# Kernel tuning notes

Measured on AMD Instinct MI355X. Metric: run time of the kernel, lower is better.

## Reference

```python
import jax, jax.numpy as jnp
import numpy as np

DIM = 256
HEADS = 8
HEAD_DIM = 32
INNER = HEADS * HEAD_DIM  # 256
B, L_AG, H, W = 2, 5, 32, 32
SEQ = H * W
POS_HID = 32


def _lin(k, fan_in, fan_out):
    kw, kb = jax.random.split(k)
    Wt = jax.random.normal(kw, (fan_in, fan_out), jnp.float32) * (fan_in ** -0.5)
    b = jax.random.normal(kb, (fan_out,), jnp.float32) * 0.01
    return Wt, b


def setup_inputs() -> dict:
    key = jax.random.key(0)
    ks = jax.random.split(key, 10)
    x = jax.random.normal(ks[0], (B, L_AG, H, W, DIM), jnp.float32)
    Wq, bq = _lin(ks[1], DIM, INNER)
    Wk, bk = _lin(ks[2], DIM, INNER)
    Wv, bv = _lin(ks[3], DIM, INNER)
    Wp1, bp1 = _lin(ks[4], 3, POS_HID)
    Wp2, bp2 = _lin(ks[5], POS_HID, HEADS)
    Ws1, bs1 = _lin(ks[6], DIM, POS_HID)
    Ws2, bs2 = _lin(ks[7], POS_HID, HEADS)
    Wo, bo = _lin(ks[8], INNER, DIM)
    Wg, bg = _lin(ks[9], 2 * DIM, DIM)
    return dict(x=x, Wq=Wq, bq=bq, Wk=Wk, bk=bk, Wv=Wv, bv=bv,
                Wp1=Wp1, bp1=bp1, Wp2=Wp2, bp2=bp2,
                Ws1=Ws1, bs1=bs1, Ws2=Ws2, bs2=bs2,
                Wo=Wo, bo=bo, Wg=Wg, bg=bg)


def _relative_positions(h, w):
    # coords: (h*w, 2), row-major (i//w, i%w) like torch meshgrid 'ij'
    yy, xx = jnp.meshgrid(jnp.arange(h), jnp.arange(w), indexing='ij')
    coords = jnp.stack([yy.reshape(-1), xx.reshape(-1)], axis=-1)  # (L,2)
    rel = (coords[:, None, :] - coords[None, :, :]).astype(jnp.float32)  # (L,L,2)
    dist = jnp.linalg.norm(rel, axis=-1, keepdims=True)  # (L,L,1)
    return jnp.concatenate([rel, dist], axis=-1)  # (L,L,3)


def reference(x, Wq, bq, Wk, bk, Wv, bv, Wp1, bp1, Wp2, bp2,
              Ws1, bs1, Ws2, bs2, Wo, bo, Wg, bg):
    b, l, h, w, c = x.shape
    bl, L = b * l, h * w
    scale = HEAD_DIM ** -0.5
    x2 = x.reshape(bl, L, c)

    q = (x2 @ Wq + bq).reshape(bl, L, HEADS, HEAD_DIM)
    k = (x2 @ Wk + bk).reshape(bl, L, HEADS, HEAD_DIM)
    v = (x2 @ Wv + bv).reshape(bl, L, HEADS, HEAD_DIM)

    scores = jnp.einsum('bihd,bjhd->bhij', q, k) * scale  # (bl,H,L,L)

    rel_pos = _relative_positions(h, w)  # (L,L,3)
    pos_w = jax.nn.relu(rel_pos @ Wp1 + bp1) @ Wp2 + bp2  # (L,L,heads)
    pos_w = jnp.transpose(pos_w, (2, 0, 1))[None]  # (1,heads,L,L)

    s = jax.nn.relu(x2 @ Ws1 + bs1) @ Ws2 + bs2  # (bl,L,heads)
    fsim = jnp.einsum('bih,bjh->bij', s, s)[:, None]  # (bl,1,L,L)

    probs = jax.nn.softmax(scores + pos_w + fsim, axis=-1)
    out = jnp.einsum('bhij,bjhd->bihd', probs, v).reshape(bl, L, INNER)
    out = out @ Wo + bo  # (bl,L,dim); dropout is identity in eval

    gate = jax.nn.sigmoid(jnp.concatenate([x2, out], axis=-1) @ Wg + bg)
    out = gate * out + (1.0 - gate) * x2
    return out.reshape(b, l, h, w, c)
```

## Files before the change

### kernel.cpp

```cpp
#include <hip/hip_runtime.h>

typedef __bf16 bf16_t;
typedef __bf16 bf16x4 __attribute__((ext_vector_type(4)));
typedef __bf16 bf16x8 __attribute__((ext_vector_type(8)));
typedef float  f32x4  __attribute__((ext_vector_type(4)));

#define HEADS 8
#define HEAD_DIM 32
#define DIM 256
#define BL 10
#define SEQ 1024
#define M_TOTAL (BL*SEQ)
#define QK_SCALE 0.17677669529663687f
#define LOG2E 1.4426950408889634f
#define SQRT_LOG2E 1.2011224087864498f
#define NPOS (63*63)

#define NCAST 2596
#define NTRANS 96
#define NPREP (NCAST + NTRANS + 16)

__device__ __forceinline__ int swz_idx(int row, int col) {
  return row*64 + (col ^ ((row & 7) << 3));
}
// ... 20 lines not shown
  if (bid < NCAST) {
    const int NX4 = M_TOTAL*DIM/4;
    const int i = bid*256 + tid;
    if (i < NX4) {
      const float4 v = ((const float4*)x)[i];
      bf16x4 o; o[0]=(bf16_t)v.x; o[1]=(bf16_t)v.y; o[2]=(bf16_t)v.z; o[3]=(bf16_t)v.w;
      *(bf16x4*)(xb + (size_t)i*4) = o;
      return;
    }
    int idx = i - NX4;
    if (idx < 8192) {
      const int m = idx >> 8, k = idx & 255;
      btall[(768 + m)*256 + k] = (bf16_t)Ws1[k*32 + m];
      return;
    }
    idx -= 8192;
    if (idx < 832) {
      bias_all[idx] = (idx < 256) ? bq[idx] : (idx < 512) ? bk[idx-256] :
                      (idx < 768) ? bv[idx-512] : (idx < 800) ? bs1[idx-768] : 0.f;
    }
    return;
  }

  if (bid < NCAST + NTRANS) {
    const int t0 = bid - NCAST;
    const int z = t0 >> 4, bi = (t0 & 15) >> 2, bj = t0 & 3;
    const float* src; bf16_t* dst;
    switch (z) {
      case 0: src = Wq;          dst = btall;          break;
      case 1: src = Wk;          dst = btall + 65536;  break;
      case 2: src = Wv;          dst = btall + 131072; break;
      case 3: src = Wo;          dst = wot;            break;
      case 4: src = Wg;          dst = wg1t;           break;
      default: src = Wg + 65536; dst = wg2t;           break;
    }
    const int tr = tid >> 4, tc = tid & 15;
    #pragma unroll
    for (int i = 0; i < 4; ++i) {
      const float4 v = *(const float4*)(src + (size_t)(bi*64 + tr + 16*i)*256 + bj*64 + tc*4);
      float* tp = &tile[tr + 16*i][tc*4];
      tp[0]=v.x; tp[1]=v.y; tp[2]=v.z; tp[3]=v.w;
    }
    __syncthreads();
    #pragma unroll
    for (int i = 0; i < 4; ++i) {
      bf16x4 o;
      #pragma unroll
      for (int e = 0; e < 4; ++e) o[e] = (bf16_t)tile[tc*4 + e][tr + 16*i];
      *(bf16x4*)(dst + (size_t)(bj*64 + tr + 16*i)*256 + bi*64 + tc*4) = o;
    }
    return;
  }

  {
    float* sm = &tile[0][0];
    float* w1 = sm; float* b1 = sm + 96; float* w2 = sm + 128; float* b2 = sm + 384;
    if (tid < 96) w1[tid] = Wp1[tid];
    if (tid < 32) b1[tid] = bp1[tid];
    w2[tid] = Wp2[tid];
    if (tid < 8)  b2[tid] = bp2[tid];
    __syncthreads();
    const int p = (bid - NCAST - NTRANS)*256 + tid;
    if (p >= NPOS) return;
    const float dy = (float)(p / 63 - 31);
    const float dx = (float)(p % 63 - 31);
    const float dist = sqrtf(dy*dy + dx*dx);
    float o[8];
    #pragma unroll
    for (int t = 0; t < 8; ++t) o[t] = b2[t];
    #pragma unroll
    for (int m = 0; m < 32; ++m) {
      float hv = fmaf(dy, w1[m], fmaf(dx, w1[32+m], fmaf(dist, w1[64+m], b1[m])));
      hv = fmaxf(hv, 0.f);
      #pragma unroll
      for (int t = 0; t < 8; ++t) o[t] = fmaf(hv, w2[m*8+t], o[t]);
    }
    #pragma unroll
    for (int t = 0; t < 8; ++t) posT[t*NPOS + p] = o[t]*LOG2E;
  }
}

__global__ __launch_bounds__(256) void qkv_kernel(
    const bf16_t* __restrict__ xb, const bf16_t* __restrict__ btall,
    const float* __restrict__ bias_all,
    bf16_t* __restrict__ qbuf, bf16_t* __restrict__ kbuf, bf16_t* __restrict__ vbuf,
    float* __restrict__ hidf)
{
  const int mt = blockIdx.x, ngb = blockIdx.y;
  const int tid = threadIdx.x;
  const int w = tid >> 6, lane = tid & 63, g = lane >> 4, l15 = lane & 15;
  const int arow = mt*64 + w*16 + l15;
  const bf16x8* Arow = (const bf16x8*)(xb + (size_t)arow*DIM);
  bf16x8 af[8];
  #pragma unroll
  for (int kc = 0; kc < 8; ++kc) af[kc] = Arow[kc*4 + g];
  const bool ishid = (ngb == 12);
  const int cmax = ishid ? 2 : 4;
  bf16_t* dst = (ngb < 4) ? qbuf : (ngb < 8) ? kbuf : vbuf;
  const int coloff = (ngb & 3) * 64;
  const float scale = (ngb < 4) ? QK_SCALE*LOG2E : 1.f;
  for (int c = 0; c < cmax; ++c) {
    const int n = ngb*64 + c*16 + l15;
    const bf16x8* Brow = (const bf16x8*)(btall + (size_t)n*DIM);
    f32x4 acc = {0.f,0.f,0.f,0.f};
    #pragma unroll
    for (int kc = 0; kc < 8; ++kc)
      acc = __builtin_amdgcn_mfma_f32_16x16x32_bf16(af[kc], Brow[kc*4+g], acc, 0, 0, 0);
    const float bvv = bias_all[n];
    #pragma unroll
    for (int r = 0; r < 4; ++r) {
      const int row = mt*64 + w*16 + g*4 + r;
      const float val = acc[r] + bvv;
      if (ishid) hidf[(size_t)row*32 + c*16 + l15] = fmaxf(val, 0.f);
      else dst[(size_t)row*DIM + coloff + c*16 + l15] = (bf16_t)(val*scale);
    }
  }
}

__global__ __launch_bounds__(256) void s2_kernel(
    const float* __restrict__ hidf, const float* __restrict__ Ws2,
    const float* __restrict__ bs2, float* __restrict__ sf)
{
  const int row = blockIdx.x*blockDim.x + threadIdx.x;
  if (row >= M_TOTAL) return;
  const float4* h4 = (const float4*)(hidf + (size_t)row*32);
  float sv[8];
  #pragma unroll
  for (int t = 0; t < 8; ++t) sv[t] = bs2[t];
  #pragma unroll
  for (int mq = 0; mq < 8; ++mq) {
    const float4 h = h4[mq];
    const float hv[4] = {h.x, h.y, h.z, h.w};
    #pragma unroll
    for (int e = 0; e < 4; ++e) {
      #pragma unroll
      for (int t = 0; t < 8; ++t) sv[t] = fmaf(hv[e], Ws2[(mq*4+e)*8+t], sv[t]);
    }
  }
  #pragma unroll
  for (int t = 0; t < 8; ++t) sf[(size_t)row*8+t] = sv[t]*SQRT_LOG2E;
}

__global__ __launch_bounds__(256) void attn_kernel(
    const bf16_t* __restrict__ qb, const bf16_t* __restrict__ kb,
    const bf16_t* __restrict__ vb, const float* __restrict__ sf,
    const float* __restrict__ posT, bf16_t* __restrict__ att)
{
  __shared__ __align__(16) bf16_t lqp[64*64];
  __shared__ __align__(16) bf16_t lk[64*64];
  __shared__ __align__(16) bf16_t lv[48*64];

  const int wg = blockIdx.x;
  const int xcd = wg & 7, within = wg >> 3;
  const int pair = xcd*10 + (within >> 4);
  const int it = within & 15;
  const int h = pair & 7, b = pair >> 3;
  const int i0 = it*64;
  const int tid = threadIdx.x;
  const int w = tid >> 6, lane = tid & 63, g = lane >> 4, l15 = lane & 15;
  const int r4 = tid >> 2, q4 = tid & 3;

  const float* posTh = posT + h*NPOS;
  int Cr[4];
  #pragma unroll
  for (int r = 0; r < 4; ++r) {
    const int irow = i0 + w*16 + g*4 + r;
    Cr[r] = ((irow >> 5) + 31)*63 + (irow & 31) + 31;
  }

  bf16x8 kreg = *(const bf16x8*)(kb + (size_t)(b*SEQ + r4)*DIM + h*HEAD_DIM + q4*8);
  bf16x8 vreg = *(const bf16x8*)(vb + (size_t)(b*SEQ + r4)*DIM + h*HEAD_DIM + q4*8);
  float4 sA, sB;
  if (tid < 64) {
    const float* sp = sf + (size_t)(b*SEQ + tid)*8;
    sA = *(const float4*)sp; sB = *(const float4*)(sp + 4);
  }
  float pf[4][4];
  #pragma unroll
  for (int c = 0; c < 4; ++c) {
    const int j = c*16 + l15;
    const int gj = (j >> 5)*63 + (j & 31);
    #pragma unroll
    for (int r = 0; r < 4; ++r) pf[c][r] = posTh[Cr[r] - gj];
  }

  for (int p = tid; p < 16*64; p += 256) {
    const int d = 32 + (p >> 6), j = p & 63;
    lv[d*64 + (j ^ ((d & 7) << 3))] = (bf16_t)((d == 32) ? 1.f : 0.f);
  }
  for (int p = tid; p < 192; p += 256) {
    const int rr = p / 3, ch = 5 + (p % 3);
    bf16x8 z;
    #pragma unroll
    for (int e = 0; e < 8; ++e) z[e] = (bf16_t)0.f;
    *(bf16x8*)&lk[swz_idx(rr, ch*8)] = z;
  }
  {
    const int grow = b*SEQ + i0 + r4;
    #pragma unroll
    for (int cc = 0; cc < 2; ++cc) {
      const int ch = q4*2 + cc;
      bf16x8 v;
      if (ch < 4) {
        v = *(const bf16x8*)(qb + (size_t)grow*DIM + h*HEAD_DIM + ch*8);
      } else if (ch == 4) {
        const float* sp = sf + (size_t)grow*8;
        #pragma unroll
        for (int e = 0; e < 8; ++e) v[e] = (bf16_t)sp[e];
      } else {
        #pragma unroll
        for (int e = 0; e < 8; ++e) v[e] = (bf16_t)0.f;
      }
      *(bf16x8*)&lqp[swz_idx(r4, ch*8)] = v;
    }
  }
  __syncthreads();

  const int qrow = w*16 + l15;
  const bf16x8 aq0 = *(const bf16x8*)&lqp[swz_idx(qrow, g*8)];
  const bf16x8 aq1 = *(const bf16x8*)&lqp[swz_idx(qrow, 32 + g*8)];

  f32x4 accO0 = {0.f,0.f,0.f,0.f}, accO1 = {0.f,0.f,0.f,0.f}, accO2 = {0.f,0.f,0.f,0.f};
  float mrow[4];
  #pragma unroll
  for (int r = 0; r < 4; ++r) mrow[r] = -1e30f;

  for (int jt = 0; jt < 16; ++jt) {
    const int j0 = jt*64;
    __syncthreads();
    *(bf16x8*)&lk[swz_idx(r4, q4*8)] = kreg;
    #pragma unroll
    for (int e = 0; e < 8; ++e) {
      const int d = q4*8 + e;
      lv[d*64 + (r4 ^ ((d & 7) << 3))] = vreg[e];
    }
    if (tid < 64) {
      bf16x8 sv;
      sv[0]=(bf16_t)sA.x; sv[1]=(bf16_t)sA.y; sv[2]=(bf16_t)sA.z; sv[3]=(bf16_t)sA.w;
      sv[4]=(bf16_t)sB.x; sv[5]=(bf16_t)sB.y; sv[6]=(bf16_t)sB.z; sv[7]=(bf16_t)sB.w;
      *(bf16x8*)&lk[swz_idx(tid, 32)] = sv;
    }
    __syncthreads();

    if (jt < 15) {
      const int grow = b*SEQ + j0 + 64 + r4;
      kreg = *(const bf16x8*)(kb + (size_t)grow*DIM + h*HEAD_DIM + q4*8);
      vreg = *(const bf16x8*)(vb + (size_t)grow*DIM + h*HEAD_DIM + q4*8);
      if (tid < 64) {
        const float* sp = sf + (size_t)(b*SEQ + j0 + 64 + tid)*8;
        sA = *(const float4*)sp; sB = *(const float4*)(sp + 4);
      }
    }

    f32x4 s4[4];
    #pragma unroll
    for (int c = 0; c < 4; ++c) {
      const int krow = c*16 + l15;
      const bf16x8 bk0 = *(const bf16x8*)&lk[swz_idx(krow, g*8)];
      const bf16x8 bk1 = *(const bf16x8*)&lk[swz_idx(krow, 32 + g*8)];
      f32x4 acc = {0.f,0.f,0.f,0.f};
      acc = __builtin_amdgcn_mfma_f32_16x16x32_bf16(aq0, bk0, acc, 0, 0, 0);
      acc = __builtin_amdgcn_mfma_f32_16x16x32_bf16(aq1, bk1, acc, 0, 0, 0);
      s4[c] = acc;
    }

    #pragma unroll
    for (int c = 0; c < 4; ++c) {
      #pragma unroll
      for (int r = 0; r < 4; ++r) s4[c][r] += pf[c][r];
    }
    if (jt < 15) {
      #pragma unroll
      for (int c = 0; c < 4; ++c) {
        const int j = j0 + 64 + c*16 + l15;
        const int gj = (j >> 5)*63 + (j & 31);
        #pragma unroll
        for (int r = 0; r < 4; ++r) pf[c][r] = posTh[Cr[r] - gj];
      }
    }

    float pmax[4];
    #pragma unroll
    for (int r = 0; r < 4; ++r)
      pmax[r] = fmaxf(fmaxf(s4[0][r], s4[1][r]), fmaxf(s4[2][r], s4[3][r]));
    #pragma unroll
    for (int mk = 1; mk <= 8; mk <<= 1) {
      #pragma unroll
      for (int r = 0; r < 4; ++r)
        pmax[r] = fmaxf(pmax[r], __shfl_xor(pmax[r], mk));
    }
    bool need = false;
    #pragma unroll
    for (int r = 0; r < 4; ++r) need = need || (pmax[r] > mrow[r] + 8.f);
    if (__any(need)) {
      #pragma unroll
      for (int r = 0; r < 4; ++r) {
        const float mn = fmaxf(mrow[r], pmax[r]);
        const float alpha = exp2f(mrow[r] - mn);
        mrow[r] = mn;
        accO0[r] *= alpha; accO1[r] *= alpha; accO2[r] *= alpha;
      }
    }
    #pragma unroll
    for (int r = 0; r < 4; ++r) {
      #pragma unroll
      for (int c = 0; c < 4; ++c) s4[c][r] = exp2f(s4[c][r] - mrow[r]);
    }

    #pragma unroll
    for (int c = 0; c < 4; ++c) {
      #pragma unroll
      for (int r = 0; r < 4; ++r)
        lqp[swz_idx(w*16 + g*4 + r, c*16 + l15)] = (bf16_t)s4[c][r];
    }

    const int prow = w*16 + l15;
    #pragma unroll
    for (int kc = 0; kc < 2; ++kc) {
      const bf16x8 ap  = *(const bf16x8*)&lqp[swz_idx(prow, kc*32 + g*8)];
      const bf16x8 bv0 = *(const bf16x8*)&lv[swz_idx(l15,      kc*32 + g*8)];
      const bf16x8 bv1 = *(const bf16x8*)&lv[swz_idx(16 + l15, kc*32 + g*8)];
      const bf16x8 bv2 = *(const bf16x8*)&lv[swz_idx(32 + l15, kc*32 + g*8)];
      accO0 = __builtin_amdgcn_mfma_f32_16x16x32_bf16(ap, bv0, accO0, 0, 0, 0);
      accO1 = __builtin_amdgcn_mfma_f32_16x16x32_bf16(ap, bv1, accO1, 0, 0, 0);
      accO2 = __builtin_amdgcn_mfma_f32_16x16x32_bf16(ap, bv2, accO2, 0, 0, 0);
    }
  }

  #pragma unroll
  for (int r = 0; r < 4; ++r) {
    const int row = b*SEQ + i0 + w*16 + g*4 + r;
    const float lsum = __shfl(accO2[r], lane & 48);
    const float inv = 1.f / lsum;
    att[(size_t)row*DIM + h*HEAD_DIM + l15]      = (bf16_t)(accO0[r]*inv);
    att[(size_t)row*DIM + h*HEAD_DIM + 16 + l15] = (bf16_t)(accO1[r]*inv);
  }
}

__global__ __launch_bounds__(256) void prjgate_kernel(
    const bf16_t* __restrict__ att, const bf16_t* __restrict__ wot,
    const float* __restrict__ bo, const bf16_t* __restrict__ xb,
    const float* __restrict__ x, const bf16_t* __restrict__ wg1t,
    const bf16_t* __restrict__ wg2t, const float* __restrict__ bg,
    float* __restrict__ outp)
{
  __shared__ __align__(16) bf16_t prjT[16*256];
  const int row0 = blockIdx.x * 16;
  const int tid = threadIdx.x;
  const int w = tid >> 6, lane = tid & 63, g = lane >> 4, l15 = lane & 15;
  const int arow = row0 + l15;

  {
    const bf16x8* Arow = (const bf16x8*)(att + (size_t)arow*DIM);
    bf16x8 afA[8];
    #pragma unroll
    for (int kc = 0; kc < 8; ++kc) afA[kc] = Arow[kc*4 + g];
    #pragma unroll
    for (int ct = 0; ct < 4; ++ct) {
      const int n = w*64 + ct*16 + l15;
      const bf16x8* Brow = (const bf16x8*)(wot + (size_t)n*DIM);
      f32x4 acc = {0.f,0.f,0.f,0.f};
      #pragma unroll
      for (int kc = 0; kc < 8; ++kc)
        acc = __builtin_amdgcn_mfma_f32_16x16x32_bf16(afA[kc], Brow[kc*4+g], acc, 0, 0, 0);
      const float bvo = bo[n];
      #pragma unroll
      for (int r = 0; r < 4; ++r)
        prjT[swz256(g*4 + r, n)] = (bf16_t)(acc[r] + bvo);
    }
  }
  __syncthreads();

  const bf16x8* A1r = (const bf16x8*)(xb + (size_t)arow*DIM);
  bf16x8 a1[8], a2[8];
  #pragma unroll
  for (int kc = 0; kc < 8; ++kc) {
    a1[kc] = A1r[kc*4 + g];
    a2[kc] = *(const bf16x8*)&prjT[swz256(l15, kc*32 + g*8)];
  }
  #pragma unroll
  for (int ct = 0; ct < 4; ++ct) {
    const int n = w*64 + ct*16 + l15;
    const bf16x8* b1 = (const bf16x8*)(wg1t + (size_t)n*DIM);
    const bf16x8* b2 = (const bf16x8*)(wg2t + (size_t)n*DIM);
    f32x4 acc = {0.f,0.f,0.f,0.f};
    #pragma unroll
    for (int kc = 0; kc < 8; ++kc)
      acc = __builtin_amdgcn_mfma_f32_16x16x32_bf16(a1[kc], b1[kc*4+g], acc, 0, 0, 0);
    #pragma unroll
    for (int kc = 0; kc < 8; ++kc)
      acc = __builtin_amdgcn_mfma_f32_16x16x32_bf16(a2[kc], b2[kc*4+g], acc, 0, 0, 0);
    const float bgv = bg[n];
    #pragma unroll
    for (int r = 0; r < 4; ++r) {
      const int grow = row0 + g*4 + r;
      const float gate = 1.f / (1.f + __expf(-(acc[r] + bgv)));
      const float pv = (float)prjT[swz256(g*4 + r, n)];
      const float xv = x[(size_t)grow*DIM + n];
      outp[(size_t)grow*DIM + n] = gate*pv + (1.f - gate)*xv;
    }
  }
}

extern "C" void kernel_launch(void* const* d_in, const int* in_sizes, int n_in,
                              void* d_out, int out_size, void* d_ws, size_t ws_size,
                              hipStream_t stream)
{
  const float* x   = (const float*)d_in[0];
  const float* Wq  = (const float*)d_in[1];
  const float* bq  = (const float*)d_in[2];
  const float* Wk  = (const float*)d_in[3];
  const float* bk  = (const float*)d_in[4];
  const float* Wv  = (const float*)d_in[5];
  const float* bv  = (const float*)d_in[6];
  const float* Wp1 = (const float*)d_in[7];
  const float* bp1 = (const float*)d_in[8];
  const float* Wp2 = (const float*)d_in[9];
  const float* bp2 = (const float*)d_in[10];
  const float* Ws1 = (const float*)d_in[11];
  const float* bs1 = (const float*)d_in[12];
  const float* Ws2 = (const float*)d_in[13];
  const float* bs2 = (const float*)d_in[14];
  const float* Wo  = (const float*)d_in[15];
  const float* bo  = (const float*)d_in[16];
  const float* Wg  = (const float*)d_in[17];
  const float* bg  = (const float*)d_in[18];

  char* ws = (char*)d_ws;
  size_t off = 0;
  auto alloc = [&](size_t bytes) {
    char* p = ws + off;
    off += (bytes + 255) & ~(size_t)255;
    return p;
  };
  bf16_t* xb    = (bf16_t*)alloc((size_t)M_TOTAL*DIM*2);
  bf16_t* qbuf  = (bf16_t*)alloc((size_t)M_TOTAL*DIM*2);
  bf16_t* kbuf  = (bf16_t*)alloc((size_t)M_TOTAL*DIM*2);
  bf16_t* vbuf  = (bf16_t*)alloc((size_t)M_TOTAL*DIM*2);
  bf16_t* att   = (bf16_t*)alloc((size_t)M_TOTAL*DIM*2);
  bf16_t* btall = (bf16_t*)alloc((size_t)800*256*2);
  bf16_t* wot   = (bf16_t*)alloc(65536*2);
  bf16_t* wg1t  = (bf16_t*)alloc(65536*2);
  bf16_t* wg2t  = (bf16_t*)alloc(65536*2);
  float*  bias_all = (float*)alloc(832*4);
  float*  hidf  = (float*)alloc((size_t)M_TOTAL*32*4);
  float*  sfb   = (float*)alloc((size_t)M_TOTAL*8*4);
  float*  posT  = (float*)alloc((size_t)HEADS*NPOS*4);
  (void)ws_size; (void)in_sizes; (void)n_in; (void)out_size;

  prep_all_kernel<<<NPREP, 256, 0, stream>>>(x, Ws1, bq, bk, bv, bs1,
                                             Wq, Wk, Wv, Wo, Wg, Wp1, bp1, Wp2, bp2,
                                             xb, btall, bias_all, wot, wg1t, wg2t, posT);
  qkv_kernel<<<dim3(M_TOTAL/64, 13), 256, 0, stream>>>(xb, btall, bias_all,
                                                       qbuf, kbuf, vbuf, hidf);
  s2_kernel<<<M_TOTAL/256, 256, 0, stream>>>(hidf, Ws2, bs2, sfb);
  attn_kernel<<<SEQ/64*HEADS*BL, 256, 0, stream>>>(qbuf, kbuf, vbuf, sfb, posT, att);
  prjgate_kernel<<<M_TOTAL/16, 256, 0, stream>>>(att, wot, bo, xb, x, wg1t, wg2t, bg,
                                                 (float*)d_out);
}
```

Baseline: 170.1 us.

## Fuse s2 projection into qkv kernel and restructure attention K/V staging

Folds the small s2 projection into the hidden-column blocks of the qkv kernel through an LDS tile, and emits the result as bf16, which removes one launch and the fp32 hidden buffer round trip. The attention kernel now loads Q and K fragments straight from global memory into registers, double-buffered across an unrolled pair of iterations, so the K tile is no longer staged in LDS. V is double-buffered in LDS so each tile needs only one barrier instead of two. The relative-position rows the block needs are cached in an LDS table rather than gathered from global memory. In exchange it uses more registers and shared memory and sets an occupancy hint of 4 blocks per CU.

```diff
diff --git a/kernel.cpp b/kernel.cpp
--- a/kernel.cpp
+++ b/kernel.cpp
@@ -126,10 +126,12 @@
 
 __global__ __launch_bounds__(256) void qkv_kernel(
     const bf16_t* __restrict__ xb, const bf16_t* __restrict__ btall,
-    const float* __restrict__ bias_all,
+    const float* __restrict__ bias_all, const float* __restrict__ Ws2,
+    const float* __restrict__ bs2,
     bf16_t* __restrict__ qbuf, bf16_t* __restrict__ kbuf, bf16_t* __restrict__ vbuf,
-    float* __restrict__ hidf)
+    bf16_t* __restrict__ sbb)
 {
+  __shared__ float hidlds[64][33];
   const int mt = blockIdx.x, ngb = blockIdx.y;
   const int tid = threadIdx.x;
   const int w = tid >> 6, lane = tid & 63, g = lane >> 4, l15 = lane & 15;
@@ -138,238 +140,215 @@
   bf16x8 af[8];
   #pragma unroll
   for (int kc = 0; kc < 8; ++kc) af[kc] = Arow[kc*4 + g];
-  const bool ishid = (ngb == 12);
-  const int cmax = ishid ? 2 : 4;
-  bf16_t* dst = (ngb < 4) ? qbuf : (ngb < 8) ? kbuf : vbuf;
-  const int coloff = (ngb & 3) * 64;
-  const float scale = (ngb < 4) ? QK_SCALE*LOG2E : 1.f;
-  for (int c = 0; c < cmax; ++c) {
-    const int n = ngb*64 + c*16 + l15;
-    const bf16x8* Brow = (const bf16x8*)(btall + (size_t)n*DIM);
-    f32x4 acc = {0.f,0.f,0.f,0.f};
-    #pragma unroll
-    for (int kc = 0; kc < 8; ++kc)
-      acc = __builtin_amdgcn_mfma_f32_16x16x32_bf16(af[kc], Brow[kc*4+g], acc, 0, 0, 0);
-    const float bvv = bias_all[n];
-    #pragma unroll
-    for (int r = 0; r < 4; ++r) {
-      const int row = mt*64 + w*16 + g*4 + r;
-      const float val = acc[r] + bvv;
-      if (ishid) hidf[(size_t)row*32 + c*16 + l15] = fmaxf(val, 0.f);
-      else dst[(size_t)row*DIM + coloff + c*16 + l15] = (bf16_t)(val*scale);
-    }
-  }
-}
-
-__global__ __launch_bounds__(256) void s2_kernel(
-    const float* __restrict__ hidf, const float* __restrict__ Ws2,
-    const float* __restrict__ bs2, float* __restrict__ sf)
-{
-  const int row = blockIdx.x*blockDim.x + threadIdx.x;
-  if (row >= M_TOTAL) return;
-  const float4* h4 = (const float4*)(hidf + (size_t)row*32);
-  float sv[8];
-  #pragma unroll
-  for (int t = 0; t < 8; ++t) sv[t] = bs2[t];
-  #pragma unroll
-  for (int mq = 0; mq < 8; ++mq) {
-    const float4 h = h4[mq];
-    const float hv[4] = {h.x, h.y, h.z, h.w};
-    #pragma unroll
-    for (int e = 0; e < 4; ++e) {
-      #pragma unroll
-      for (int t = 0; t < 8; ++t) sv[t] = fmaf(hv[e], Ws2[(mq*4+e)*8+t], sv[t]);
-    }
-  }
-  #pragma unroll
-  for (int t = 0; t < 8; ++t) sf[(size_t)row*8+t] = sv[t]*SQRT_LOG2E;
-}
-
-__global__ __launch_bounds__(256) void attn_kernel(
+  if (ngb < 12) {
+    bf16_t* dst = (ngb < 4) ? qbuf : (ngb < 8) ? kbuf : vbuf;
+    const int coloff = (ngb & 3) * 64;
+    const float scale = (ngb < 4) ? QK_SCALE*LOG2E : 1.f;
+    for (int c = 0; c < 4; ++c) {
+      const int n = ngb*64 + c*16 + l15;
+      const bf16x8* Brow = (const bf16x8*)(btall + (size_t)n*DIM);
+      f32x4 acc = {0.f,0.f,0.f,0.f};
+      #pragma unroll
+      for (int kc = 0; kc < 8; ++kc)
+        acc = __builtin_amdgcn_mfma_f32_16x16x32_bf16(af[kc], Brow[kc*4+g], acc, 0, 0, 0);
+      const float bvv = bias_all[n];
+      #pragma unroll
+      for (int r = 0; r < 4; ++r) {
+        const int row = mt*64 + w*16 + g*4 + r;
+        dst[(size_t)row*DIM + coloff + c*16 + l15] = (bf16_t)((acc[r] + bvv)*scale);
+      }
+    }
+  } else {
+    for (int c = 0; c < 2; ++c) {
+      const int n = 768 + c*16 + l15;
+      const bf16x8* Brow = (const bf16x8*)(btall + (size_t)n*DIM);
+      f32x4 acc = {0.f,0.f,0.f,0.f};
+      #pragma unroll
+      for (int kc = 0; kc < 8; ++kc)
+        acc = __builtin_amdgcn_mfma_f32_16x16x32_bf16(af[kc], Brow[kc*4+g], acc, 0, 0, 0);
+      const float bvv = bias_all[n];
+      #pragma unroll
+      for (int r = 0; r < 4; ++r)
+        hidlds[w*16 + g*4 + r][c*16 + l15] = fmaxf(acc[r] + bvv, 0.f);
+    }
+    __syncthreads();
+    if (tid < 64) {
+      float sv[8];
+      #pragma unroll
+      for (int t = 0; t < 8; ++t) sv[t] = bs2[t];
+      #pragma unroll
+      for (int m = 0; m < 32; ++m) {
+        const float hv = hidlds[tid][m];
+        #pragma unroll
+        for (int t = 0; t < 8; ++t) sv[t] = fmaf(hv, Ws2[m*8+t], sv[t]);
+      }
+      bf16x8 o;
+      #pragma unroll
+      for (int t = 0; t < 8; ++t) o[t] = (bf16_t)(sv[t]*SQRT_LOG2E);
+      *(bf16x8*)(sbb + (size_t)(mt*64 + tid)*8) = o;
+    }
+  }
+}
+
+__global__ __launch_bounds__(256, 4) void attn_kernel(
     const bf16_t* __restrict__ qb, const bf16_t* __restrict__ kb,
-    const bf16_t* __restrict__ vb, const float* __restrict__ sf,
+    const bf16_t* __restrict__ vb, const bf16_t* __restrict__ sbb,
     const float* __restrict__ posT, bf16_t* __restrict__ att)
 {
-  __shared__ __align__(16) bf16_t lqp[64*64];
-  __shared__ __align__(16) bf16_t lk[64*64];
-  __shared__ __align__(16) bf16_t lv[48*64];
+  __shared__ __align__(16) bf16_t lp[64*64];
+  __shared__ __align__(16) bf16_t lv[2][48*64];
+  __shared__ float ptab[33*63];
 
   const int wg = blockIdx.x;
   const int xcd = wg & 7, within = wg >> 3;
   const int pair = xcd*10 + (within >> 4);
   const int it = within & 15;
   const int h = pair & 7, b = pair >> 3;
-  const int i0 = it*64;
+  const int i0 = it*64, iy0 = it*2;
   const int tid = threadIdx.x;
   const int w = tid >> 6, lane = tid & 63, g = lane >> 4, l15 = lane & 15;
   const int r4 = tid >> 2, q4 = tid & 3;
 
-  const float* posTh = posT + h*NPOS;
-  int Cr[4];
-  #pragma unroll
-  for (int r = 0; r < 4; ++r) {
-    const int irow = i0 + w*16 + g*4 + r;
-    Cr[r] = ((irow >> 5) + 31)*63 + (irow & 31) + 31;
-  }
-
-  bf16x8 kreg = *(const bf16x8*)(kb + (size_t)(b*SEQ + r4)*DIM + h*HEAD_DIM + q4*8);
+  for (int p = tid; p < 33*63; p += 256) {
+    const int rr = p / 63, cc = p - rr*63;
+    ptab[p] = posT[h*NPOS + (iy0 + rr)*63 + cc];
+  }
+  if (tid < 128) lv[tid >> 6][32*64 + (tid & 63)] = (bf16_t)1.f;
+  for (int p = tid; p < 2*15*64; p += 256) {
+    const int buf = p / (15*64), rem = p - buf*15*64;
+    const int d = 33 + (rem >> 6), j = rem & 63;
+    lv[buf][d*64 + (j ^ ((d & 7) << 3))] = (bf16_t)0.f;
+  }
+
+  const int qrow = b*SEQ + i0 + w*16 + l15;
+  const bf16x8 aq0 = *(const bf16x8*)(qb + (size_t)qrow*DIM + h*HEAD_DIM + g*8);
+  bf16x8 aq1 = {};
+  if (g == 0) aq1 = *(const bf16x8*)(sbb + (size_t)qrow*8);
+
   bf16x8 vreg = *(const bf16x8*)(vb + (size_t)(b*SEQ + r4)*DIM + h*HEAD_DIM + q4*8);
-  float4 sA, sB;
-  if (tid < 64) {
-    const float* sp = sf + (size_t)(b*SEQ + tid)*8;
-    sA = *(const float4*)sp; sB = *(const float4*)(sp + 4);
-  }
-  float pf[4][4];
-  #pragma unroll
-  for (int c = 0; c < 4; ++c) {
-    const int j = c*16 + l15;
-    const int gj = (j >> 5)*63 + (j & 31);
-    #pragma unroll
-    for (int r = 0; r < 4; ++r) pf[c][r] = posTh[Cr[r] - gj];
-  }
-
-  for (int p = tid; p < 16*64; p += 256) {
-    const int d = 32 + (p >> 6), j = p & 63;
-    lv[d*64 + (j ^ ((d & 7) << 3))] = (bf16_t)((d == 32) ? 1.f : 0.f);
-  }
-  for (int p = tid; p < 192; p += 256) {
-    const int rr = p / 3, ch = 5 + (p % 3);
-    bf16x8 z;
-    #pragma unroll
-    for (int e = 0; e < 8; ++e) z[e] = (bf16_t)0.f;
-    *(bf16x8*)&lk[swz_idx(rr, ch*8)] = z;
-  }
-  {
-    const int grow = b*SEQ + i0 + r4;
-    #pragma unroll
-    for (int cc = 0; cc < 2; ++cc) {
-      const int ch = q4*2 + cc;
-      bf16x8 v;
-      if (ch < 4) {
-        v = *(const bf16x8*)(qb + (size_t)grow*DIM + h*HEAD_DIM + ch*8);
-      } else if (ch == 4) {
-        const float* sp = sf + (size_t)grow*8;
-        #pragma unroll
-        for (int e = 0; e < 8; ++e) v[e] = (bf16_t)sp[e];
-      } else {
-        #pragma unroll
-        for (int e = 0; e < 8; ++e) v[e] = (bf16_t)0.f;
-      }
-      *(bf16x8*)&lqp[swz_idx(r4, ch*8)] = v;
-    }
-  }
-  __syncthreads();
-
-  const int qrow = w*16 + l15;
-  const bf16x8 aq0 = *(const bf16x8*)&lqp[swz_idx(qrow, g*8)];
-  const bf16x8 aq1 = *(const bf16x8*)&lqp[swz_idx(qrow, 32 + g*8)];
+  bf16x8 akA[4], akB[4], ak1[4];
+  #pragma unroll
+  for (int c = 0; c < 4; ++c) { ak1[c] = bf16x8{}; }
+  #pragma unroll
+  for (int c = 0; c < 4; ++c)
+    akA[c] = *(const bf16x8*)(kb + (size_t)(b*SEQ + c*16 + l15)*DIM + h*HEAD_DIM + g*8);
 
   f32x4 accO0 = {0.f,0.f,0.f,0.f}, accO1 = {0.f,0.f,0.f,0.f}, accO2 = {0.f,0.f,0.f,0.f};
   float mrow[4];
   #pragma unroll
   for (int r = 0; r < 4; ++r) mrow[r] = -1e30f;
 
-  for (int jt = 0; jt < 16; ++jt) {
-    const int j0 = jt*64;
-    __syncthreads();
-    *(bf16x8*)&lk[swz_idx(r4, q4*8)] = kreg;
-    #pragma unroll
-    for (int e = 0; e < 8; ++e) {
-      const int d = q4*8 + e;
-      lv[d*64 + (r4 ^ ((d & 7) << 3))] = vreg[e];
-    }
-    if (tid < 64) {
-      bf16x8 sv;
-      sv[0]=(bf16_t)sA.x; sv[1]=(bf16_t)sA.y; sv[2]=(bf16_t)sA.z; sv[3]=(bf16_t)sA.w;
-      sv[4]=(bf16_t)sB.x; sv[5]=(bf16_t)sB.y; sv[6]=(bf16_t)sB.z; sv[7]=(bf16_t)sB.w;
-      *(bf16x8*)&lk[swz_idx(tid, 32)] = sv;
-    }
-    __syncthreads();
-
-    if (jt < 15) {
-      const int grow = b*SEQ + j0 + 64 + r4;
-      kreg = *(const bf16x8*)(kb + (size_t)grow*DIM + h*HEAD_DIM + q4*8);
-      vreg = *(const bf16x8*)(vb + (size_t)grow*DIM + h*HEAD_DIM + q4*8);
-      if (tid < 64) {
-        const float* sp = sf + (size_t)(b*SEQ + j0 + 64 + tid)*8;
-        sA = *(const float4*)sp; sB = *(const float4*)(sp + 4);
-      }
-    }
-
-    f32x4 s4[4];
-    #pragma unroll
-    for (int c = 0; c < 4; ++c) {
-      const int krow = c*16 + l15;
-      const bf16x8 bk0 = *(const bf16x8*)&lk[swz_idx(krow, g*8)];
-      const bf16x8 bk1 = *(const bf16x8*)&lk[swz_idx(krow, 32 + g*8)];
-      f32x4 acc = {0.f,0.f,0.f,0.f};
-      acc = __builtin_amdgcn_mfma_f32_16x16x32_bf16(aq0, bk0, acc, 0, 0, 0);
-      acc = __builtin_amdgcn_mfma_f32_16x16x32_bf16(aq1, bk1, acc, 0, 0, 0);
-      s4[c] = acc;
-    }
-
-    #pragma unroll
-    for (int c = 0; c < 4; ++c) {
-      #pragma unroll
-      for (int r = 0; r < 4; ++r) s4[c][r] += pf[c][r];
-    }
-    if (jt < 15) {
-      #pragma unroll
-      for (int c = 0; c < 4; ++c) {
-        const int j = j0 + 64 + c*16 + l15;
-        const int gj = (j >> 5)*63 + (j & 31);
-        #pragma unroll
-        for (int r = 0; r < 4; ++r) pf[c][r] = posTh[Cr[r] - gj];
-      }
-    }
-
-    float pmax[4];
-    #pragma unroll
-    for (int r = 0; r < 4; ++r)
-      pmax[r] = fmaxf(fmaxf(s4[0][r], s4[1][r]), fmaxf(s4[2][r], s4[3][r]));
-    #pragma unroll
-    for (int mk = 1; mk <= 8; mk <<= 1) {
-      #pragma unroll
-      for (int r = 0; r < 4; ++r)
-        pmax[r] = fmaxf(pmax[r], __shfl_xor(pmax[r], mk));
-    }
-    bool need = false;
-    #pragma unroll
-    for (int r = 0; r < 4; ++r) need = need || (pmax[r] > mrow[r] + 8.f);
-    if (__any(need)) {
-      #pragma unroll
-      for (int r = 0; r < 4; ++r) {
-        const float mn = fmaxf(mrow[r], pmax[r]);
-        const float alpha = exp2f(mrow[r] - mn);
-        mrow[r] = mn;
-        accO0[r] *= alpha; accO1[r] *= alpha; accO2[r] *= alpha;
-      }
-    }
-    #pragma unroll
-    for (int r = 0; r < 4; ++r) {
-      #pragma unroll
-      for (int c = 0; c < 4; ++c) s4[c][r] = exp2f(s4[c][r] - mrow[r]);
-    }
-
-    #pragma unroll
-    for (int c = 0; c < 4; ++c) {
-      #pragma unroll
-      for (int r = 0; r < 4; ++r)
-        lqp[swz_idx(w*16 + g*4 + r, c*16 + l15)] = (bf16_t)s4[c][r];
-    }
-
-    const int prow = w*16 + l15;
-    #pragma unroll
-    for (int kc = 0; kc < 2; ++kc) {
-      const bf16x8 ap  = *(const bf16x8*)&lqp[swz_idx(prow, kc*32 + g*8)];
-      const bf16x8 bv0 = *(const bf16x8*)&lv[swz_idx(l15,      kc*32 + g*8)];
-      const bf16x8 bv1 = *(const bf16x8*)&lv[swz_idx(16 + l15, kc*32 + g*8)];
-      const bf16x8 bv2 = *(const bf16x8*)&lv[swz_idx(32 + l15, kc*32 + g*8)];
-      accO0 = __builtin_amdgcn_mfma_f32_16x16x32_bf16(ap, bv0, accO0, 0, 0, 0);
-      accO1 = __builtin_amdgcn_mfma_f32_16x16x32_bf16(ap, bv1, accO1, 0, 0, 0);
-      accO2 = __builtin_amdgcn_mfma_f32_16x16x32_bf16(ap, bv2, accO2, 0, 0, 0);
-    }
-  }
+#define ATTN_ITER(JT, AKC, AKN)                                                        \
+  {                                                                                    \
+    const int j0 = (JT)*64;                                                            \
+    const int pb = (JT) & 1;                                                           \
+                                                             \
+    _Pragma("unroll")                                                                  \
+    for (int e = 0; e < 8; ++e) {                                                      \
+      const int d = q4*8 + e;                                                          \
+      lv[pb][d*64 + (r4 ^ ((d & 7) << 3))] = vreg[e];                                  \
+    }                                                                                  \
+    __syncthreads();                                                                   \
+                                      \
+    if (g == 0) {                                                                      \
+      _Pragma("unroll")                                                                \
+      for (int c = 0; c < 4; ++c)                                                      \
+        ak1[c] = *(const bf16x8*)(sbb + (size_t)(b*SEQ + j0 + c*16 + l15)*8);          \
+    }                                                                                  \
+                                                         \
+    {                                                                                  \
+      const int jn = (JT) < 15 ? j0 + 64 : j0;                                         \
+      vreg = *(const bf16x8*)(vb + (size_t)(b*SEQ + jn + r4)*DIM + h*HEAD_DIM + q4*8); \
+    }                                                                                  \
+                           \
+    f32x4 s4[4];                                                                       \
+    _Pragma("unroll")                                                                  \
+    for (int c = 0; c < 4; ++c) {                                                      \
+      f32x4 acc = {0.f,0.f,0.f,0.f};                                                   \
+      acc = __builtin_amdgcn_mfma_f32_16x16x32_bf16(aq0, AKC[c], acc, 0, 0, 0);        \
+      acc = __builtin_amdgcn_mfma_f32_16x16x32_bf16(aq1, ak1[c], acc, 0, 0, 0);        \
+      s4[c] = acc;                                                                     \
+    }                                                                                  \
+                                               \
+    {                                                                                  \
+      const int jn = (JT) < 15 ? j0 + 64 : j0;                                         \
+      _Pragma("unroll")                                                                \
+      for (int c = 0; c < 4; ++c)                                                      \
+        AKN[c] = *(const bf16x8*)(kb + (size_t)(b*SEQ + jn + c*16 + l15)*DIM           \
+                                  + h*HEAD_DIM + g*8);                                 \
+    }                                                                                  \
+                                                                            \
+    {                                                                                  \
+      const int ib = i0 + w*16 + g*4;                                                  \
+      _Pragma("unroll")                                                                \
+      for (int r = 0; r < 4; ++r) {                                                    \
+        const int rbase = ((ib + r) >> 5) - iy0 + 31;                                  \
+        const int ixr = (ib + r) & 31;                                                 \
+        _Pragma("unroll")                                                              \
+        for (int c = 0; c < 4; ++c) {                                                  \
+          const int j = j0 + c*16 + l15;                                               \
+          s4[c][r] += ptab[(rbase - (j >> 5))*63 + (ixr - (j & 31) + 31)];             \
+        }                                                                              \
+      }                                                                                \
+    }                                                                                  \
+                                    \
+    {                                                                                  \
+      float pmax[4];                                                                   \
+      _Pragma("unroll")                                                                \
+      for (int r = 0; r < 4; ++r)                                                      \
+        pmax[r] = fmaxf(fmaxf(s4[0][r], s4[1][r]), fmaxf(s4[2][r], s4[3][r]));         \
+      _Pragma("unroll")                                                                \
+      for (int mk = 1; mk <= 8; mk <<= 1) {                                            \
+        _Pragma("unroll")                                                              \
+        for (int r = 0; r < 4; ++r)                                                    \
+          pmax[r] = fmaxf(pmax[r], __shfl_xor(pmax[r], mk));                           \
+      }                                                                                \
+      bool need = false;                                                               \
+      _Pragma("unroll")                                                                \
+      for (int r = 0; r < 4; ++r) need = need || (pmax[r] > mrow[r] + 8.f);            \
+      if (__any(need)) {                                                               \
+        _Pragma("unroll")                                                              \
+        for (int r = 0; r < 4; ++r) {                                                  \
+          const float mn = fmaxf(mrow[r], pmax[r]);                                    \
+          const float alpha = exp2f(mrow[r] - mn);                                     \
+          mrow[r] = mn;                                                                \
+          accO0[r] *= alpha; accO1[r] *= alpha; accO2[r] *= alpha;                     \
+        }                                                                              \
+      }                                                                                \
+      _Pragma("unroll")                                                                \
+      for (int r = 0; r < 4; ++r) {                                                    \
+        _Pragma("unroll")                                                              \
+        for (int c = 0; c < 4; ++c) s4[c][r] = exp2f(s4[c][r] - mrow[r]);              \
+      }                                                                                \
+    }                                                                                  \
+                                                       \
+    _Pragma("unroll")                                                                  \
+    for (int c = 0; c < 4; ++c) {                                                      \
+      _Pragma("unroll")                                                                \
+      for (int r = 0; r < 4; ++r)                                                      \
+        lp[swz_idx(w*16 + g*4 + r, c*16 + l15)] = (bf16_t)s4[c][r];                    \
+    }                                                                                  \
+                                                                               \
+    {                                                                                  \
+      const int prow = w*16 + l15;                                                     \
+      _Pragma("unroll")                                                                \
+      for (int kc = 0; kc < 2; ++kc) {                                                 \
+        const bf16x8 ap  = *(const bf16x8*)&lp[swz_idx(prow, kc*32 + g*8)];            \
+        const bf16x8 bv0 = *(const bf16x8*)&lv[pb][swz_idx(l15,      kc*32 + g*8)];    \
+        const bf16x8 bv1 = *(const bf16x8*)&lv[pb][swz_idx(16 + l15, kc*32 + g*8)];    \
+        const bf16x8 bv2 = *(const bf16x8*)&lv[pb][swz_idx(32 + l15, kc*32 + g*8)];    \
+        accO0 = __builtin_amdgcn_mfma_f32_16x16x32_bf16(ap, bv0, accO0, 0, 0, 0);      \
+        accO1 = __builtin_amdgcn_mfma_f32_16x16x32_bf16(ap, bv1, accO1, 0, 0, 0);      \
+        accO2 = __builtin_amdgcn_mfma_f32_16x16x32_bf16(ap, bv2, accO2, 0, 0, 0);      \
+      }                                                                                \
+    }                                                                                  \
+  }
+
+  for (int jt = 0; jt < 16; jt += 2) {
+    ATTN_ITER(jt,     akA, akB)
+    ATTN_ITER(jt + 1, akB, akA)
+  }
+#undef ATTN_ITER
 
   #pragma unroll
   for (int r = 0; r < 4; ++r) {
@@ -487,18 +466,16 @@
   bf16_t* wg1t  = (bf16_t*)alloc(65536*2);
   bf16_t* wg2t  = (bf16_t*)alloc(65536*2);
   float*  bias_all = (float*)alloc(832*4);
-  float*  hidf  = (float*)alloc((size_t)M_TOTAL*32*4);
-  float*  sfb   = (float*)alloc((size_t)M_TOTAL*8*4);
+  bf16_t* sbb   = (bf16_t*)alloc((size_t)M_TOTAL*8*2);
   float*  posT  = (float*)alloc((size_t)HEADS*NPOS*4);
   (void)ws_size; (void)in_sizes; (void)n_in; (void)out_size;
 
   prep_all_kernel<<<NPREP, 256, 0, stream>>>(x, Ws1, bq, bk, bv, bs1,
                                              Wq, Wk, Wv, Wo, Wg, Wp1, bp1, Wp2, bp2,
                                              xb, btall, bias_all, wot, wg1t, wg2t, posT);
-  qkv_kernel<<<dim3(M_TOTAL/64, 13), 256, 0, stream>>>(xb, btall, bias_all,
-                                                       qbuf, kbuf, vbuf, hidf);
-  s2_kernel<<<M_TOTAL/256, 256, 0, stream>>>(hidf, Ws2, bs2, sfb);
-  attn_kernel<<<SEQ/64*HEADS*BL, 256, 0, stream>>>(qbuf, kbuf, vbuf, sfb, posT, att);
+  qkv_kernel<<<dim3(M_TOTAL/64, 13), 256, 0, stream>>>(xb, btall, bias_all, Ws2, bs2,
+                                                       qbuf, kbuf, vbuf, sbb);
+  attn_kernel<<<SEQ/64*HEADS*BL, 256, 0, stream>>>(qbuf, kbuf, vbuf, sbb, posT, att);
   prjgate_kernel<<<M_TOTAL/16, 256, 0, stream>>>(att, wot, bo, xb, x, wg1t, wg2t, bg,
                                                  (float*)d_out);
 }
```

Result: slower. 215.8 us (+26.9%).

## Fuse s2 into qkv kernel, stage pos table in LDS, transpose attention MFMA

Applied to the files above, without the earlier changes.

Folds the second similarity MLP layer into the qkv kernel's hidden block through LDS and stores the result as bf16, which removes a kernel launch and the fp32 hidden round trip. The attention kernel now loads a 33x63 slice of the position table into shared memory per block instead of gathering it from global memory on every tile. It also swaps the QK MFMA operands so each lane holds one query row, turning the row-max into two shuffles, and loads Q directly from global memory. The cost is extra LDS use, which may lower occupancy, and bf16 rounding of the similarity features.

```diff
diff --git a/kernel.cpp b/kernel.cpp
--- a/kernel.cpp
+++ b/kernel.cpp
@@ -126,10 +126,12 @@
 
 __global__ __launch_bounds__(256) void qkv_kernel(
     const bf16_t* __restrict__ xb, const bf16_t* __restrict__ btall,
-    const float* __restrict__ bias_all,
+    const float* __restrict__ bias_all, const float* __restrict__ Ws2,
+    const float* __restrict__ bs2,
     bf16_t* __restrict__ qbuf, bf16_t* __restrict__ kbuf, bf16_t* __restrict__ vbuf,
-    float* __restrict__ hidf)
+    bf16_t* __restrict__ sbb)
 {
+  __shared__ float hidlds[64][33];
   const int mt = blockIdx.x, ngb = blockIdx.y;
   const int tid = threadIdx.x;
   const int w = tid >> 6, lane = tid & 63, g = lane >> 4, l15 = lane & 15;
@@ -138,136 +140,106 @@
   bf16x8 af[8];
   #pragma unroll
   for (int kc = 0; kc < 8; ++kc) af[kc] = Arow[kc*4 + g];
-  const bool ishid = (ngb == 12);
-  const int cmax = ishid ? 2 : 4;
-  bf16_t* dst = (ngb < 4) ? qbuf : (ngb < 8) ? kbuf : vbuf;
-  const int coloff = (ngb & 3) * 64;
-  const float scale = (ngb < 4) ? QK_SCALE*LOG2E : 1.f;
-  for (int c = 0; c < cmax; ++c) {
-    const int n = ngb*64 + c*16 + l15;
-    const bf16x8* Brow = (const bf16x8*)(btall + (size_t)n*DIM);
-    f32x4 acc = {0.f,0.f,0.f,0.f};
-    #pragma unroll
-    for (int kc = 0; kc < 8; ++kc)
-      acc = __builtin_amdgcn_mfma_f32_16x16x32_bf16(af[kc], Brow[kc*4+g], acc, 0, 0, 0);
-    const float bvv = bias_all[n];
-    #pragma unroll
-    for (int r = 0; r < 4; ++r) {
-      const int row = mt*64 + w*16 + g*4 + r;
-      const float val = acc[r] + bvv;
-      if (ishid) hidf[(size_t)row*32 + c*16 + l15] = fmaxf(val, 0.f);
-      else dst[(size_t)row*DIM + coloff + c*16 + l15] = (bf16_t)(val*scale);
-    }
-  }
-}
-
-__global__ __launch_bounds__(256) void s2_kernel(
-    const float* __restrict__ hidf, const float* __restrict__ Ws2,
-    const float* __restrict__ bs2, float* __restrict__ sf)
-{
-  const int row = blockIdx.x*blockDim.x + threadIdx.x;
-  if (row >= M_TOTAL) return;
-  const float4* h4 = (const float4*)(hidf + (size_t)row*32);
-  float sv[8];
-  #pragma unroll
-  for (int t = 0; t < 8; ++t) sv[t] = bs2[t];
-  #pragma unroll
-  for (int mq = 0; mq < 8; ++mq) {
-    const float4 h = h4[mq];
-    const float hv[4] = {h.x, h.y, h.z, h.w};
-    #pragma unroll
-    for (int e = 0; e < 4; ++e) {
-      #pragma unroll
-      for (int t = 0; t < 8; ++t) sv[t] = fmaf(hv[e], Ws2[(mq*4+e)*8+t], sv[t]);
-    }
-  }
-  #pragma unroll
-  for (int t = 0; t < 8; ++t) sf[(size_t)row*8+t] = sv[t]*SQRT_LOG2E;
+  if (ngb < 12) {
+    bf16_t* dst = (ngb < 4) ? qbuf : (ngb < 8) ? kbuf : vbuf;
+    const int coloff = (ngb & 3) * 64;
+    const float scale = (ngb < 4) ? QK_SCALE*LOG2E : 1.f;
+    for (int c = 0; c < 4; ++c) {
+      const int n = ngb*64 + c*16 + l15;
+      const bf16x8* Brow = (const bf16x8*)(btall + (size_t)n*DIM);
+      f32x4 acc = {0.f,0.f,0.f,0.f};
+      #pragma unroll
+      for (int kc = 0; kc < 8; ++kc)
+        acc = __builtin_amdgcn_mfma_f32_16x16x32_bf16(af[kc], Brow[kc*4+g], acc, 0, 0, 0);
+      const float bvv = bias_all[n];
+      #pragma unroll
+      for (int r = 0; r < 4; ++r) {
+        const int row = mt*64 + w*16 + g*4 + r;
+        dst[(size_t)row*DIM + coloff + c*16 + l15] = (bf16_t)((acc[r] + bvv)*scale);
+      }
+    }
+  } else {
+    for (int c = 0; c < 2; ++c) {
+      const int n = 768 + c*16 + l15;
+      const bf16x8* Brow = (const bf16x8*)(btall + (size_t)n*DIM);
+      f32x4 acc = {0.f,0.f,0.f,0.f};
+      #pragma unroll
+      for (int kc = 0; kc < 8; ++kc)
+        acc = __builtin_amdgcn_mfma_f32_16x16x32_bf16(af[kc], Brow[kc*4+g], acc, 0, 0, 0);
+      const float bvv = bias_all[n];
+      #pragma unroll
+      for (int r = 0; r < 4; ++r)
+        hidlds[w*16 + g*4 + r][c*16 + l15] = fmaxf(acc[r] + bvv, 0.f);
+    }
+    __syncthreads();
+    if (tid < 64) {
+      float sv[8];
+      #pragma unroll
+      for (int t = 0; t < 8; ++t) sv[t] = bs2[t];
+      #pragma unroll
+      for (int m = 0; m < 32; ++m) {
+        const float hv = hidlds[tid][m];
+        #pragma unroll
+        for (int t = 0; t < 8; ++t) sv[t] = fmaf(hv, Ws2[m*8+t], sv[t]);
+      }
+      bf16x8 o;
+      #pragma unroll
+      for (int t = 0; t < 8; ++t) o[t] = (bf16_t)(sv[t]*SQRT_LOG2E);
+      *(bf16x8*)(sbb + (size_t)(mt*64 + tid)*8) = o;
+    }
+  }
 }
 
 __global__ __launch_bounds__(256) void attn_kernel(
     const bf16_t* __restrict__ qb, const bf16_t* __restrict__ kb,
-    const bf16_t* __restrict__ vb, const float* __restrict__ sf,
+    const bf16_t* __restrict__ vb, const bf16_t* __restrict__ sbb,
     const float* __restrict__ posT, bf16_t* __restrict__ att)
 {
-  __shared__ __align__(16) bf16_t lqp[64*64];
   __shared__ __align__(16) bf16_t lk[64*64];
   __shared__ __align__(16) bf16_t lv[48*64];
+  __shared__ __align__(16) bf16_t lp[64*64];
+  __shared__ float ptab[33*63];
 
   const int wg = blockIdx.x;
   const int xcd = wg & 7, within = wg >> 3;
   const int pair = xcd*10 + (within >> 4);
   const int it = within & 15;
   const int h = pair & 7, b = pair >> 3;
-  const int i0 = it*64;
+  const int i0 = it*64, iy0 = it*2;
   const int tid = threadIdx.x;
   const int w = tid >> 6, lane = tid & 63, g = lane >> 4, l15 = lane & 15;
   const int r4 = tid >> 2, q4 = tid & 3;
 
-  const float* posTh = posT + h*NPOS;
-  int Cr[4];
-  #pragma unroll
-  for (int r = 0; r < 4; ++r) {
-    const int irow = i0 + w*16 + g*4 + r;
-    Cr[r] = ((irow >> 5) + 31)*63 + (irow & 31) + 31;
-  }
-
-  bf16x8 kreg = *(const bf16x8*)(kb + (size_t)(b*SEQ + r4)*DIM + h*HEAD_DIM + q4*8);
-  bf16x8 vreg = *(const bf16x8*)(vb + (size_t)(b*SEQ + r4)*DIM + h*HEAD_DIM + q4*8);
-  float4 sA, sB;
-  if (tid < 64) {
-    const float* sp = sf + (size_t)(b*SEQ + tid)*8;
-    sA = *(const float4*)sp; sB = *(const float4*)(sp + 4);
-  }
-  float pf[4][4];
-  #pragma unroll
-  for (int c = 0; c < 4; ++c) {
-    const int j = c*16 + l15;
-    const int gj = (j >> 5)*63 + (j & 31);
-    #pragma unroll
-    for (int r = 0; r < 4; ++r) pf[c][r] = posTh[Cr[r] - gj];
-  }
-
+  for (int p = tid; p < 33*63; p += 256) {
+    const int rr = p / 63, cc = p - rr*63;
+    ptab[p] = posT[h*NPOS + (iy0 + rr)*63 + cc];
+  }
   for (int p = tid; p < 16*64; p += 256) {
     const int d = 32 + (p >> 6), j = p & 63;
     lv[d*64 + (j ^ ((d & 7) << 3))] = (bf16_t)((d == 32) ? 1.f : 0.f);
   }
   for (int p = tid; p < 192; p += 256) {
     const int rr = p / 3, ch = 5 + (p % 3);
-    bf16x8 z;
-    #pragma unroll
-    for (int e = 0; e < 8; ++e) z[e] = (bf16_t)0.f;
+    bf16x8 z = {};
     *(bf16x8*)&lk[swz_idx(rr, ch*8)] = z;
   }
-  {
-    const int grow = b*SEQ + i0 + r4;
-    #pragma unroll
-    for (int cc = 0; cc < 2; ++cc) {
-      const int ch = q4*2 + cc;
-      bf16x8 v;
-      if (ch < 4) {
-        v = *(const bf16x8*)(qb + (size_t)grow*DIM + h*HEAD_DIM + ch*8);
-      } else if (ch == 4) {
-        const float* sp = sf + (size_t)grow*8;
-        #pragma unroll
-        for (int e = 0; e < 8; ++e) v[e] = (bf16_t)sp[e];
-      } else {
-        #pragma unroll
-        for (int e = 0; e < 8; ++e) v[e] = (bf16_t)0.f;
-      }
-      *(bf16x8*)&lqp[swz_idx(r4, ch*8)] = v;
-    }
-  }
-  __syncthreads();
-
-  const int qrow = w*16 + l15;
-  const bf16x8 aq0 = *(const bf16x8*)&lqp[swz_idx(qrow, g*8)];
-  const bf16x8 aq1 = *(const bf16x8*)&lqp[swz_idx(qrow, 32 + g*8)];
+
+  const int qrow = b*SEQ + i0 + w*16 + l15;
+  const bf16x8 aq0 = *(const bf16x8*)(qb + (size_t)qrow*DIM + h*HEAD_DIM + g*8);
+  bf16x8 aq1 = {};
+  if (g == 0) aq1 = *(const bf16x8*)(sbb + (size_t)qrow*8);
+
+  const int iq = i0 + w*16 + l15;
+  const int rbase_i = (iq >> 5) - iy0 + 31;
+  const int ixr = iq & 31;
+
+  bf16x8 kreg = *(const bf16x8*)(kb + (size_t)(b*SEQ + r4)*DIM + h*HEAD_DIM + q4*8);
+  bf16x8 vreg = *(const bf16x8*)(vb + (size_t)(b*SEQ + r4)*DIM + h*HEAD_DIM + q4*8);
+  bf16x8 sreg = {};
+  if (tid < 64) sreg = *(const bf16x8*)(sbb + (size_t)(b*SEQ + tid)*8);
 
   f32x4 accO0 = {0.f,0.f,0.f,0.f}, accO1 = {0.f,0.f,0.f,0.f}, accO2 = {0.f,0.f,0.f,0.f};
-  float mrow[4];
-  #pragma unroll
-  for (int r = 0; r < 4; ++r) mrow[r] = -1e30f;
+  float mrow = -1e30f;
 
   for (int jt = 0; jt < 16; ++jt) {
     const int j0 = jt*64;
@@ -278,90 +250,74 @@
       const int d = q4*8 + e;
       lv[d*64 + (r4 ^ ((d & 7) << 3))] = vreg[e];
     }
-    if (tid < 64) {
-      bf16x8 sv;
-      sv[0]=(bf16_t)sA.x; sv[1]=(bf16_t)sA.y; sv[2]=(bf16_t)sA.z; sv[3]=(bf16_t)sA.w;
-      sv[4]=(bf16_t)sB.x; sv[5]=(bf16_t)sB.y; sv[6]=(bf16_t)sB.z; sv[7]=(bf16_t)sB.w;
-      *(bf16x8*)&lk[swz_idx(tid, 32)] = sv;
-    }
+    if (tid < 64) *(bf16x8*)&lk[swz_idx(tid, 32)] = sreg;
     __syncthreads();
 
     if (jt < 15) {
-      const int grow = b*SEQ + j0 + 64 + r4;
-      kreg = *(const bf16x8*)(kb + (size_t)grow*DIM + h*HEAD_DIM + q4*8);
-      vreg = *(const bf16x8*)(vb + (size_t)grow*DIM + h*HEAD_DIM + q4*8);
-      if (tid < 64) {
-        const float* sp = sf + (size_t)(b*SEQ + j0 + 64 + tid)*8;
-        sA = *(const float4*)sp; sB = *(const float4*)(sp + 4);
+      const int grow = b*SEQ + j0 + 64;
+      kreg = *(const bf16x8*)(kb + (size_t)(grow + r4)*DIM + h*HEAD_DIM + q4*8);
+      vreg = *(const bf16x8*)(vb + (size_t)(grow + r4)*DIM + h*HEAD_DIM + q4*8);
+      if (tid < 64) sreg = *(const bf16x8*)(sbb + (size_t)(grow + tid)*8);
+    }
+
+    f32x4 s4[4];
+    #pragma unroll
+    for (int c = 0; c < 4; ++c) {
+      const bf16x8 kf0 = *(const bf16x8*)&lk[swz_idx(c*16 + l15, g*8)];
+      const bf16x8 kf1 = *(const bf16x8*)&lk[swz_idx(c*16 + l15, 32 + g*8)];
+      f32x4 acc = {0.f,0.f,0.f,0.f};
+      acc = __builtin_amdgcn_mfma_f32_16x16x32_bf16(kf0, aq0, acc, 0, 0, 0);
+      acc = __builtin_amdgcn_mfma_f32_16x16x32_bf16(kf1, aq1, acc, 0, 0, 0);
+      s4[c] = acc;
+    }
+
+    #pragma unroll
+    for (int c = 0; c < 4; ++c) {
+      #pragma unroll
+      for (int r = 0; r < 4; ++r) {
+        const int jl = c*16 + g*4 + r;
+        const int jy = jt*2 + (jl >> 5);
+        const int jx = jl & 31;
+        s4[c][r] += ptab[(rbase_i - jy)*63 + (ixr - jx + 31)];
       }
     }
 
-    f32x4 s4[4];
-    #pragma unroll
-    for (int c = 0; c < 4; ++c) {
-      const int krow = c*16 + l15;
-      const bf16x8 bk0 = *(const bf16x8*)&lk[swz_idx(krow, g*8)];
-      const bf16x8 bk1 = *(const bf16x8*)&lk[swz_idx(krow, 32 + g*8)];
-      f32x4 acc = {0.f,0.f,0.f,0.f};
-      acc = __builtin_amdgcn_mfma_f32_16x16x32_bf16(aq0, bk0, acc, 0, 0, 0);
-      acc = __builtin_amdgcn_mfma_f32_16x16x32_bf16(aq1, bk1, acc, 0, 0, 0);
-      s4[c] = acc;
-    }
-
-    #pragma unroll
-    for (int c = 0; c < 4; ++c) {
-      #pragma unroll
-      for (int r = 0; r < 4; ++r) s4[c][r] += pf[c][r];
-    }
-    if (jt < 15) {
-      #pragma unroll
-      for (int c = 0; c < 4; ++c) {
-        const int j = j0 + 64 + c*16 + l15;
-        const int gj = (j >> 5)*63 + (j & 31);
-        #pragma unroll
-        for (int r = 0; r < 4; ++r) pf[c][r] = posTh[Cr[r] - gj];
+    float m16 = s4[0][0];
+    #pragma unroll
+    for (int c = 0; c < 4; ++c) {
+      #pragma unroll
+      for (int r = 0; r < 4; ++r) m16 = fmaxf(m16, s4[c][r]);
+    }
+    m16 = fmaxf(m16, __shfl_xor(m16, 16));
+    m16 = fmaxf(m16, __shfl_xor(m16, 32));
+    if (__any(m16 > mrow + 8.f)) {
+      const float mn = fmaxf(mrow, m16);
+      const float alpha = exp2f(mrow - mn);
+      mrow = mn;
+      #pragma unroll
+      for (int r = 0; r < 4; ++r) {
+        const float aO = __shfl(alpha, g*16 + g*4 + r);
+        accO0[r] *= aO; accO1[r] *= aO; accO2[r] *= aO;
       }
     }
-
-    float pmax[4];
-    #pragma unroll
-    for (int r = 0; r < 4; ++r)
-      pmax[r] = fmaxf(fmaxf(s4[0][r], s4[1][r]), fmaxf(s4[2][r], s4[3][r]));
-    #pragma unroll
-    for (int mk = 1; mk <= 8; mk <<= 1) {
-      #pragma unroll
-      for (int r = 0; r < 4; ++r)
-        pmax[r] = fmaxf(pmax[r], __shfl_xor(pmax[r], mk));
-    }
-    bool need = false;
-    #pragma unroll
-    for (int r = 0; r < 4; ++r) need = need || (pmax[r] > mrow[r] + 8.f);
-    if (__any(need)) {
-      #pragma unroll
-      for (int r = 0; r < 4; ++r) {
-        const float mn = fmaxf(mrow[r], pmax[r]);
-        const float alpha = exp2f(mrow[r] - mn);
-        mrow[r] = mn;
-        accO0[r] *= alpha; accO1[r] *= alpha; accO2[r] *= alpha;
-      }
-    }
-    #pragma unroll
-    for (int r = 0; r < 4; ++r) {
-      #pragma unroll
-      for (int c = 0; c < 4; ++c) s4[c][r] = exp2f(s4[c][r] - mrow[r]);
-    }
-
-    #pragma unroll
-    for (int c = 0; c < 4; ++c) {
-      #pragma unroll
-      for (int r = 0; r < 4; ++r)
-        lqp[swz_idx(w*16 + g*4 + r, c*16 + l15)] = (bf16_t)s4[c][r];
+    #pragma unroll
+    for (int c = 0; c < 4; ++c) {
+      #pragma unroll
+      for (int r = 0; r < 4; ++r) s4[c][r] = exp2f(s4[c][r] - mrow);
+    }
+
+    #pragma unroll
+    for (int c = 0; c < 4; ++c) {
+      bf16x4 o;
+      #pragma unroll
+      for (int r = 0; r < 4; ++r) o[r] = (bf16_t)s4[c][r];
+      *(bf16x4*)&lp[swz_idx(w*16 + l15, c*16 + g*4)] = o;
     }
 
     const int prow = w*16 + l15;
     #pragma unroll
     for (int kc = 0; kc < 2; ++kc) {
-      const bf16x8 ap  = *(const bf16x8*)&lqp[swz_idx(prow, kc*32 + g*8)];
+      const bf16x8 ap  = *(const bf16x8*)&lp[swz_idx(prow, kc*32 + g*8)];
       const bf16x8 bv0 = *(const bf16x8*)&lv[swz_idx(l15,      kc*32 + g*8)];
       const bf16x8 bv1 = *(const bf16x8*)&lv[swz_idx(16 + l15, kc*32 + g*8)];
       const bf16x8 bv2 = *(const bf16x8*)&lv[swz_idx(32 + l15, kc*32 + g*8)];
@@ -487,18 +443,16 @@
   bf16_t* wg1t  = (bf16_t*)alloc(65536*2);
   bf16_t* wg2t  = (bf16_t*)alloc(65536*2);
   float*  bias_all = (float*)alloc(832*4);
-  float*  hidf  = (float*)alloc((size_t)M_TOTAL*32*4);
-  float*  sfb   = (float*)alloc((size_t)M_TOTAL*8*4);
+  bf16_t* sbb   = (bf16_t*)alloc((size_t)M_TOTAL*8*2);
   float*  posT  = (float*)alloc((size_t)HEADS*NPOS*4);
   (void)ws_size; (void)in_sizes; (void)n_in; (void)out_size;
 
   prep_all_kernel<<<NPREP, 256, 0, stream>>>(x, Ws1, bq, bk, bv, bs1,
                                              Wq, Wk, Wv, Wo, Wg, Wp1, bp1, Wp2, bp2,
                                              xb, btall, bias_all, wot, wg1t, wg2t, posT);
-  qkv_kernel<<<dim3(M_TOTAL/64, 13), 256, 0, stream>>>(xb, btall, bias_all,
-                                                       qbuf, kbuf, vbuf, hidf);
-  s2_kernel<<<M_TOTAL/256, 256, 0, stream>>>(hidf, Ws2, bs2, sfb);
-  attn_kernel<<<SEQ/64*HEADS*BL, 256, 0, stream>>>(qbuf, kbuf, vbuf, sfb, posT, att);
+  qkv_kernel<<<dim3(M_TOTAL/64, 13), 256, 0, stream>>>(xb, btall, bias_all, Ws2, bs2,
+                                                       qbuf, kbuf, vbuf, sbb);
+  attn_kernel<<<SEQ/64*HEADS*BL, 256, 0, stream>>>(qbuf, kbuf, vbuf, sbb, posT, att);
   prjgate_kernel<<<M_TOTAL/16, 256, 0, stream>>>(att, wot, bo, xb, x, wg1t, wg2t, bg,
                                                  (float*)d_out);
 }
```

Result: faster. 150.9 us (-11.3%).
